# Optimization experiments

Measured on AMD Instinct MI355X. Metric: run time of the kernel, lower is better.

Reference implementation:

```python
import jax, jax.numpy as jnp
import numpy as np

B, S, D, L, H = 2, 2048, 2048, 3, 16
DH = D // H
BLOCK = 16
NA = 64
Q = NA * BLOCK
KV = S + Q
VOCAB = 32000
MASK_ID = 31999
GAMMA = 7.0
EPS = 1e-6


def _rope(x, pos):
    # x: [B,H,T,DH], pos: [B,T]
    half = DH // 2
    inv = 1.0 / (10000.0 ** (jnp.arange(half, dtype=jnp.float32) / half))
    ang = pos[:, None, :, None].astype(jnp.float32) * inv  # [B,1,T,half]
    c, s = jnp.cos(ang), jnp.sin(ang)
    x1, x2 = x[..., :half], x[..., half:]
    return jnp.concatenate([x1 * c - x2 * s, x2 * c + x1 * s], axis=-1)


def setup_inputs() -> dict:
    key = jax.random.key(0)
    ks = jax.random.split(key, 12)
    w = lambda k, shp: 0.02 * jax.random.normal(k, shp, jnp.float32)
    return {
        'input_ids': jax.random.randint(ks[0], (B, S), 0, VOCAB, dtype=jnp.int32),
        'hidden_states': jax.random.normal(ks[1], (L, B, S, D), jnp.float32),
        'loss_mask': jnp.ones((B, S), jnp.int32),
        'lm_head_weight': w(ks[2], (VOCAB, D)),
        'norm_weight': jnp.ones((D,), jnp.float32),
        'anchor_positions': jnp.sort(jax.random.randint(ks[3], (B, NA), 0, S - BLOCK, dtype=jnp.int32), axis=-1),
        'ctx_proj_w': w(ks[4], (D, L * D)),
        'embed_table': w(ks[5], (VOCAB, D)),
        'wq': w(ks[6], (D, D)),
        'wk': w(ks[7], (D, D)),
        'wv': w(ks[8], (D, D)),
        'wo': w(ks[9], (D, D)),
    }


def reference(input_ids, hidden_states, loss_mask, lm_head_weight, norm_weight,
              anchor_positions, ctx_proj_w, embed_table, wq, wk, wv, wo):
    # --- context feature: concat L target-layer hiddens, project to D ---
    ctx_cat = jnp.transpose(hidden_states, (1, 2, 0, 3)).reshape(B, S, L * D)
    ctx = jnp.einsum('bsf,df->bsd', ctx_cat, ctx_proj_w)

    # --- position ids (context: 0..S-1; draft block i starts at anchor_i) ---
    ctx_pos = jnp.broadcast_to(jnp.arange(S, dtype=jnp.int32), (B, S))
    draft_pos = (anchor_positions[:, :, None] + jnp.arange(BLOCK, dtype=jnp.int32)[None, None, :]).reshape(B, Q)

    # --- draft input (anchor token + MASKs) and labels ---
    off = jnp.arange(Q, dtype=jnp.int32) % BLOCK                       # [Q]
    anchor_per_tok = jnp.repeat(anchor_positions, BLOCK, axis=1)       # [B,Q]
    anchor_tok = jnp.take_along_axis(input_ids, anchor_positions, axis=1)
    draft_ids = jnp.where(off[None, :] == 0, jnp.repeat(anchor_tok, BLOCK, axis=1), MASK_ID)
    labels = jnp.where(off[None, :] == 0, -100,
                       jnp.take_along_axis(input_ids, anchor_per_tok + off[None, :], axis=1))

    # --- block-causal mask: [B,Q,KV] ---
    qi = jnp.arange(Q, dtype=jnp.int32)
    ki = jnp.arange(KV, dtype=jnp.int32)
    qb = qi // BLOCK                                                   # [Q]
    apos = anchor_positions[:, qb]                                     # [B,Q]
    ctx_vis = (ki[None, None, :] < S) & (ki[None, None, :] < apos[:, :, None])
    kb = (ki - S) // BLOCK
    draft_vis = (ki >= S)[None, :] & (qb[:, None] == kb[None, :])      # [Q,KV]
    mask = ctx_vis | draft_vis[None]                                   # [B,Q,KV]

    # --- single RoPE attention layer: draft queries over [context; draft] ---
    emb = embed_table[draft_ids]                                       # [B,Q,D]
    x_kv = jnp.concatenate([ctx, emb], axis=1)                         # [B,KV,D]
    pos_kv = jnp.concatenate([ctx_pos, draft_pos], axis=1)             # [B,KV]
    q = _rope((emb @ wq.T).reshape(B, Q, H, DH).transpose(0, 2, 1, 3), draft_pos)
    k = _rope((x_kv @ wk.T).reshape(B, KV, H, DH).transpose(0, 2, 1, 3), pos_kv)
    v = (x_kv @ wv.T).reshape(B, KV, H, DH).transpose(0, 2, 1, 3)
    scores = jnp.einsum('bhqd,bhkd->bhqk', q, k) / np.float32(np.sqrt(DH))
    scores = jnp.where(mask[:, None], scores, jnp.float32(-1e30))
    attn = jax.nn.softmax(scores, axis=-1)
    out = jnp.einsum('bhqk,bhkd->bhqd', attn, v).transpose(0, 2, 1, 3).reshape(B, Q, D) @ wo.T
    hidden = emb + out

    # --- RMSNorm + LM head ---
    hidden = hidden * jax.lax.rsqrt(jnp.mean(hidden * hidden, -1, keepdims=True) + EPS) * norm_weight
    logits = hidden @ lm_head_weight.T                                 # [B,Q,VOCAB]

    # --- decay-weighted CE loss + accuracy ---
    logp = jax.nn.log_softmax(logits, axis=-1)
    lab = jnp.where(labels < 0, 0, labels)
    nll = -jnp.take_along_axis(logp, lab[..., None], axis=-1)[..., 0]
    valid = labels != -100
    offf = off.astype(jnp.float32)
    decay = jnp.where(off == 0, 0.0, jnp.exp(-(offf - 1.0) / GAMMA))   # [Q]
    w = decay[None, :] * valid.astype(jnp.float32)
    loss = jnp.sum(nll * w) / jnp.maximum(jnp.sum(w), 1e-6)
    preds = jnp.argmax(logits, axis=-1).astype(labels.dtype)
    acc = jnp.sum((preds == labels) & valid) / jnp.maximum(jnp.sum(valid), 1)
    return loss, acc.astype(jnp.float32)
```

## Files before the change

### kernel.cpp

```cpp
#include <hip/hip_runtime.h>

#define B_ 2
#define S_ 2048
#define D_ 2048
#define L_ 3
#define H_ 16
#define DH_ 128
#define BLK_ 16
#define NA_ 64
#define Q_ 1024
#define KV_ 3072
#define VOCAB_ 32000
#define MASK_ID_ 31999
#define NTOK_ (B_*Q_)
#define VTILES_ (VOCAB_/128)

typedef __attribute__((ext_vector_type(8))) short bf16x8;
typedef __attribute__((ext_vector_type(4))) float f32x4;
typedef const __attribute__((address_space(1))) void* gptr_t;
typedef __attribute__((address_space(3))) void* lptr_t;

__device__ inline unsigned short f2bf(float x) {
  unsigned int u = __float_as_uint(x);
  unsigned int r = (u + 0x7fff + ((u >> 16) & 1)) >> 16;
  return (unsigned short)r;
}
__device__ inline float bf2f(unsigned short u) {
  return __uint_as_float(((unsigned int)u) << 16);
}

__global__ void k_meta(const int* __restrict__ ids, const int* __restrict__ anchors,
                       int* __restrict__ dids, int* __restrict__ dpos, int* __restrict__ labels) {
  int t = blockIdx.x * 256 + threadIdx.x;
  if (t >= NTOK_) return;
  int b = t >> 10, qi = t & 1023;
  int a = qi >> 4, off = qi & 15;
  int ap = anchors[b * NA_ + a];
  dpos[t] = ap + off;
  dids[t] = (off == 0) ? ids[b * S_ + ap] : MASK_ID_;
  labels[t] = (off == 0) ? -100 : ids[b * S_ + ap + off];
}

__global__ void k_cvt(const float* __restrict__ in, unsigned short* __restrict__ out, int n4) {
  int i = blockIdx.x * 256 + threadIdx.x;
  if (i >= n4) return;
  float4 v = ((const float4*)in)[i];
  ushort4 o;
  o.x = f2bf(v.x); o.y = f2bf(v.y); o.z = f2bf(v.z); o.w = f2bf(v.w);
  ((ushort4*)out)[i] = o;
}

__global__ void k_cvt_ctx(const float* __restrict__ hs, unsigned short* __restrict__ out) {
  int bi = blockIdx.x;
  int l = bi % 3, row = bi / 3;
  const float4* src = (const float4*)(hs + ((size_t)l * B_ * S_ + row) * (size_t)D_);
  ushort4* dst = (ushort4*)(out + (size_t)row * (3 * D_) + (size_t)l * D_);
  for (int i = threadIdx.x; i < D_ / 4; i += 256) {
    float4 v = src[i];
    ushort4 o;
    o.x = f2bf(v.x); o.y = f2bf(v.y); o.z = f2bf(v.z); o.w = f2bf(v.w);
    dst[i] = o;
  }
}

__global__ void k_gather(const float* __restrict__ table, const int* __restrict__ dids,
                         unsigned short* __restrict__ x_kv) {
  int row = blockIdx.x;
  int b = row >> 10, qi = row & 1023;
  const float4* src = (const float4*)(table + (size_t)dids[row] * D_);
  ushort4* dst = (ushort4*)(x_kv + ((size_t)b * KV_ + S_ + qi) * D_);
  for (int i = threadIdx.x; i < D_ / 4; i += 256) {
    float4 v = src[i];
    ushort4 o;
    o.x = f2bf(v.x); o.y = f2bf(v.y); o.z = f2bf(v.z); o.w = f2bf(v.w);
    dst[i] = o;
  }
}

template <int CMODE, int MAP>
__global__ __launch_bounds__(256) void k_mfma_bt(
    const unsigned short* __restrict__ A, const unsigned short* __restrict__ Bw,
    float* __restrict__ Cf, unsigned short* __restrict__ Cb,
    int M, int N, int K, int adivlog, long long abump, int cdivlog, long long cbump,
    const int* __restrict__ labels, float* __restrict__ pm, float* __restrict__ ps,
    int* __restrict__ pbi, float* __restrict__ plab) {
  __shared__ unsigned short As[128 * 32];
  __shared__ unsigned short Bs[128 * 32];
  int bx, by;
  if (MAP == 0) {
    int ntn = N >> 7;
    bx = blockIdx.x % ntn, by = blockIdx.x / ntn;
  } else {
    int per = gridDim.x >> 3;
    int wgid = (blockIdx.x & 7) * per + (blockIdx.x >> 3);
    int ntm = M >> 7;
    by = wgid % ntm, bx = wgid / ntm;
  }
  int rowbase = by << 7, colbase = bx << 7;
  int tid = threadIdx.x, lane = tid & 63, w = tid >> 6;
  int wr = w >> 1, wc = w & 1;
  int lo = lane & 15, hi = lane >> 4;

  f32x4 acc[4][4];
#pragma unroll
  for (int m = 0; m < 4; ++m)
#pragma unroll
    for (int n = 0; n < 4; ++n) acc[m][n] = (f32x4){0.f, 0.f, 0.f, 0.f};

  for (int kt = 0; kt < K; kt += 32) {
#pragma unroll
    for (int i = 0; i < 2; ++i) {
      int seg = i * 4 + w;
      int rloc = seg * 16 + (lane >> 2);
      int kcol = kt + ((lane & 3) << 3);
      int ra = rowbase + rloc;
      long long aoff = (long long)ra * K + (long long)(ra >> adivlog) * abump + kcol;
      __builtin_amdgcn_global_load_lds((gptr_t)(A + aoff), (lptr_t)(As + seg * 512), 16, 0, 0);
      int rb = colbase + rloc;
      long long boff = (long long)rb * K + kcol;
      __builtin_amdgcn_global_load_lds((gptr_t)(Bw + boff), (lptr_t)(Bs + seg * 512), 16, 0, 0);
    }
    __syncthreads();
    bf16x8 af[4], bfv[4];
#pragma unroll
    for (int m = 0; m < 4; ++m) {
      int row = wr * 64 + m * 16 + lo;
      af[m] = *(const bf16x8*)(As + row * 32 + (hi << 3));
    }
#pragma unroll
    for (int n = 0; n < 4; ++n) {
      int row = wc * 64 + n * 16 + lo;
      bfv[n] = *(const bf16x8*)(Bs + row * 32 + (hi << 3));
    }
#pragma unroll
    for (int m = 0; m < 4; ++m)
#pragma unroll
      for (int n = 0; n < 4; ++n)
        acc[m][n] = __builtin_amdgcn_mfma_f32_16x16x32_bf16(af[m], bfv[n], acc[m][n], 0, 0, 0);
    __syncthreads();
  }

  if (CMODE == 0 || CMODE == 1) {
#pragma unroll
    for (int m = 0; m < 4; ++m)
#pragma unroll
      for (int n = 0; n < 4; ++n)
#pragma unroll
        for (int r4 = 0; r4 < 4; ++r4) {
          int row = rowbase + wr * 64 + m * 16 + hi * 4 + r4;
          int col = colbase + wc * 64 + n * 16 + lo;
          size_t addr = (size_t)row * N + (size_t)(row >> cdivlog) * cbump + col;
          if (CMODE == 0) Cf[addr] = acc[m][n][r4];
          else Cb[addr] = f2bf(acc[m][n][r4]);
        }
  } else if (CMODE == 3) {
#pragma unroll
    for (int m = 0; m < 4; ++m)
#pragma unroll
      for (int n = 0; n < 4; ++n)
#pragma unroll
        for (int r4 = 0; r4 < 4; ++r4) {
          int row = rowbase + wr * 64 + m * 16 + hi * 4 + r4;
          int col = colbase + wc * 64 + n * 16 + lo;
          int bb = row >= KV_;
          int kv = row - bb * KV_;
          size_t addr = ((size_t)(bb * H_ + (col >> 7)) * 128 + (col & 127)) * KV_ + kv;
          Cb[addr] = f2bf(acc[m][n][r4]);
        }
  } else {
    float* f = (float*)As;
    int* ii = (int*)Bs;
    if (tid < 128) { f[640 + tid] = -3.0e38f; ii[256 + tid] = labels[rowbase + tid]; }
    __syncthreads();
#pragma unroll
    for (int m = 0; m < 4; ++m)
#pragma unroll
      for (int r4 = 0; r4 < 4; ++r4) {
        int trow = wr * 64 + m * 16 + hi * 4 + r4;
        float mx = acc[m][0][r4];
        int arg = colbase + wc * 64 + 0 * 16 + lo;
#pragma unroll
        for (int n = 1; n < 4; ++n) {
          float v = acc[m][n][r4];
          int c = colbase + wc * 64 + n * 16 + lo;
          if (v > mx || (v == mx && c < arg)) { mx = v; arg = c; }
        }
#pragma unroll
        for (int d = 1; d < 16; d <<= 1) {
          float om = __shfl_xor(mx, d);
          int oc = __shfl_xor(arg, d);
          if (om > mx || (om == mx && oc < arg)) { mx = om; arg = oc; }
        }
        if (lo == 0) { f[wc * 128 + trow] = mx; ii[wc * 128 + trow] = arg; }
      }
    __syncthreads();
    if (tid < 128) {
      float a = f[tid], b = f[128 + tid];
      int aa = ii[tid], bb = ii[128 + tid];
      float g; int ga;
      if (b > a || (b == a && bb < aa)) { g = b; ga = bb; } else { g = a; ga = aa; }
      f[512 + tid] = g; ii[384 + tid] = ga;
    }
    __syncthreads();
#pragma unroll
    for (int m = 0; m < 4; ++m)
#pragma unroll
      for (int r4 = 0; r4 < 4; ++r4) {
        int trow = wr * 64 + m * 16 + hi * 4 + r4;
        float gm = f[512 + trow];
        float s = 0.f;
#pragma unroll
        for (int n = 0; n < 4; ++n) s += __expf(acc[m][n][r4] - gm);
#pragma unroll
        for (int d = 1; d < 16; d <<= 1) s += __shfl_xor(s, d);
        if (lo == 0) f[256 + wc * 128 + trow] = s;
        int lab = ii[256 + trow];
        int rel = lab - colbase - wc * 64;
        if (rel >= 0 && rel < 64 && (rel & 15) == lo) {
#pragma unroll
          for (int n = 0; n < 4; ++n)
            if ((rel >> 4) == n) f[640 + trow] = acc[m][n][r4];
        }
      }
    __syncthreads();
    if (tid < 128) {
      int grow = rowbase + tid;
      size_t p = (size_t)grow * VTILES_ + bx;
      pm[p] = f[512 + tid];
      ps[p] = f[256 + tid] + f[256 + 128 + tid];
      pbi[p] = ii[384 + tid];
      plab[p] = f[640 + tid];
    }
  }
}

__global__ void k_rope(unsigned short* __restrict__ x, const int* __restrict__ dpos, int mode) {
  int idx = blockIdx.x * 256 + threadIdx.x;
  int j = idx & 63;
  int h = (idx >> 6) & 15;
  int row = idx >> 10;
  int pos;
  if (mode == 0) {
    if (row >= NTOK_) return;
    pos = dpos[row];
  } else {
    if (row >= B_ * KV_) return;
    int b = row / KV_, kvi = row % KV_;
    pos = (kvi < S_) ? kvi : dpos[b * Q_ + (kvi - S_)];
  }
  float inv = expf(-(float)j * (9.210340371976184f / 64.f));
  float ang = (float)pos * inv;
  float c = cosf(ang), s = sinf(ang);
  unsigned short* p = x + (size_t)row * D_ + h * DH_ + j;
  float x1 = bf2f(p[0]), x2 = bf2f(p[64]);
  p[0] = f2bf(x1 * c - x2 * s);
  p[64] = f2bf(x2 * c + x1 * s);
}

__global__ __launch_bounds__(256) void k_attn_mfma(
    const unsigned short* __restrict__ qb, const unsigned short* __restrict__ kb,
    const unsigned short* __restrict__ vt, const int* __restrict__ anchors,
    unsigned short* __restrict__ ob) {
  __shared__ __align__(16) unsigned short P_all[4][16 * 40];
  int w = threadIdx.x >> 6, lane = threadIdx.x & 63;
  int blk = blockIdx.x * 4 + w;
  int h = blk & 15, a = (blk >> 4) & 63, b = blk >> 10;
  int ql = lane & 15, p = lane >> 4;
  int apos = anchors[b * NA_ + a];
  unsigned short* P = P_all[w];

  const unsigned short* qbase = qb + ((size_t)(b * Q_ + a * 16 + ql)) * D_ + h * DH_;
  bf16x8 qf[4];
#pragma unroll
  for (int ks = 0; ks < 4; ++ks)
    qf[ks] = *(const bf16x8*)(qbase + ks * 32 + p * 8);

  const unsigned short* kbb = kb + (size_t)b * KV_ * D_ + h * DH_;
  const unsigned short* vtb = vt + ((size_t)(b * H_ + h)) * 128 * KV_;

  f32x4 o[8];
#pragma unroll
  for (int nt = 0; nt < 8; ++nt) o[nt] = (f32x4){0.f, 0.f, 0.f, 0.f};
  float mrun = -3.0e38f, lrun = 0.f;

  int ncx = (apos + 31) >> 5;
  const float scl = 0.08838834764831845f;

  for (int t = 0; t <= ncx; ++t) {
    int ktb = (t < ncx) ? (t << 5) : (S_ + a * 16);
    int rem = apos - (t << 5);
    int vc = (t < ncx) ? (rem < 32 ? rem : 32) : 16;
    float s[2][4];
#pragma unroll
    for (int g = 0; g < 2; ++g) {
      if (g * 16 < vc) {
        f32x4 accs = (f32x4){0.f, 0.f, 0.f, 0.f};
        const unsigned short* krow = kbb + (size_t)(ktb + g * 16 + ql) * D_;
#pragma unroll
        for (int ks = 0; ks < 4; ++ks) {
          bf16x8 kf = *(const bf16x8*)(krow + ks * 32 + p * 8);
          accs = __builtin_amdgcn_mfma_f32_16x16x32_bf16(kf, qf[ks], accs, 0, 0, 0);
        }
#pragma unroll
        for (int r = 0; r < 4; ++r) {
          int kl = g * 16 + p * 4 + r;
          s[g][r] = (kl < vc) ? accs[r] * scl : -3.0e38f;
        }
      } else {
#pragma unroll
        for (int r = 0; r < 4; ++r) s[g][r] = -3.0e38f;
      }
    }
    float mt = s[0][0];
#pragma unroll
    for (int g = 0; g < 2; ++g)
#pragma unroll
      for (int r = 0; r < 4; ++r) mt = fmaxf(mt, s[g][r]);
    mt = fmaxf(mt, __shfl_xor(mt, 16));
    mt = fmaxf(mt, __shfl_xor(mt, 32));
    float mnew = fmaxf(mrun, mt);
    float corr = __expf(mrun - mnew);
    float psum = 0.f;
#pragma unroll
    for (int g = 0; g < 2; ++g) {
      float p0 = __expf(s[g][0] - mnew), p1 = __expf(s[g][1] - mnew);
      float p2 = __expf(s[g][2] - mnew), p3 = __expf(s[g][3] - mnew);
      psum += p0 + p1 + p2 + p3;
      ushort2 w0, w1;
      w0.x = f2bf(p0); w0.y = f2bf(p1); w1.x = f2bf(p2); w1.y = f2bf(p3);
      int eo = ql * 40 + g * 16 + p * 4;
      *(ushort2*)(P + eo) = w0;
      *(ushort2*)(P + eo + 2) = w1;
    }
    psum += __shfl_xor(psum, 16);
    psum += __shfl_xor(psum, 32);
    lrun = lrun * corr + psum;
    mrun = mnew;
    float cr[4];
#pragma unroll
    for (int r = 0; r < 4; ++r) cr[r] = __shfl(corr, p * 4 + r);
#pragma unroll
    for (int nt = 0; nt < 8; ++nt)
#pragma unroll
      for (int r = 0; r < 4; ++r) o[nt][r] *= cr[r];
    bf16x8 pf = *(const bf16x8*)(P + ql * 40 + p * 8);
#pragma unroll
    for (int nt = 0; nt < 8; ++nt) {
      bf16x8 vf = *(const bf16x8*)(vtb + (size_t)(nt * 16 + ql) * KV_ + ktb + p * 8);
      o[nt] = __builtin_amdgcn_mfma_f32_16x16x32_bf16(pf, vf, o[nt], 0, 0, 0);
    }
  }
  float lq[4];
#pragma unroll
  for (int r = 0; r < 4; ++r) lq[r] = 1.f / __shfl(lrun, p * 4 + r);
  unsigned short* obase = ob + ((size_t)(b * Q_ + a * 16)) * D_ + h * DH_;
#pragma unroll
  for (int nt = 0; nt < 8; ++nt)
#pragma unroll
    for (int r = 0; r < 4; ++r)
      obase[(size_t)(p * 4 + r) * D_ + nt * 16 + ql] = f2bf(o[nt][r] * lq[r]);
}

__global__ void k_rmsnorm(const unsigned short* __restrict__ x_kv, const float* __restrict__ proj,
                          const float* __restrict__ nw, unsigned short* __restrict__ outp) {
  int row = blockIdx.x;
  int b = row >> 10, qi = row & 1023;
  const unsigned short* emb = x_kv + ((size_t)b * KV_ + S_ + qi) * D_;
  const float* pr = proj + (size_t)row * D_;
  __shared__ float red[256];
  float h[8];
  float ssum = 0.f;
#pragma unroll
  for (int i = 0; i < 8; ++i) {
    int d = threadIdx.x + i * 256;
    h[i] = bf2f(emb[d]) + pr[d];
    ssum += h[i] * h[i];
  }
  red[threadIdx.x] = ssum;
  __syncthreads();
  for (int s = 128; s; s >>= 1) {
    if (threadIdx.x < s) red[threadIdx.x] += red[threadIdx.x + s];
    __syncthreads();
  }
  float scale = rsqrtf(red[0] / (float)D_ + 1e-6f);
#pragma unroll
  for (int i = 0; i < 8; ++i) {
    int d = threadIdx.x + i * 256;
    outp[(size_t)row * D_ + d] = f2bf(h[i] * scale * nw[d]);
  }
}

__global__ void k_combine(const float* __restrict__ pm, const float* __restrict__ ps,
                          const int* __restrict__ pbi, const float* __restrict__ plab,
                          const int* __restrict__ labels, float* __restrict__ ts) {
  int t = blockIdx.x * 256 + threadIdx.x;
  if (t >= NTOK_) return;
  const float* pmr = pm + (size_t)t * VTILES_;
  const float* psr = ps + (size_t)t * VTILES_;
  const int* pbir = pbi + (size_t)t * VTILES_;
  const float* plabr = plab + (size_t)t * VTILES_;
  float M = -3.0e38f; int bi = 0;
  for (int x = 0; x < VTILES_; ++x) {
    float v = pmr[x];
    if (v > M) { M = v; bi = pbir[x]; }
  }
  float ssum = 0.f, labl = -3.0e38f;
  for (int x = 0; x < VTILES_; ++x) {
    ssum += psr[x] * __expf(pmr[x] - M);
    labl = fmaxf(labl, plabr[x]);
  }
  float lse = M + logf(ssum);
  int lab = labels[t];
  int off = t & 15;
  float valid = (lab != -100) ? 1.f : 0.f;
  float w = (off == 0) ? 0.f : __expf(-(float)(off - 1) / 7.0f);
  w *= valid;
  float nll = (lab != -100) ? (lse - labl) : 0.f;
  float correct = (valid > 0.f && bi == lab) ? 1.f : 0.f;
  ts[t * 4 + 0] = nll * w;
  ts[t * 4 + 1] = w;
  ts[t * 4 + 2] = correct;
  ts[t * 4 + 3] = valid;
}

__global__ void k_finalize(const float* __restrict__ ts, float* __restrict__ out) {
  __shared__ float r0[256], r1[256], r2[256], r3[256];
  int tid = threadIdx.x;
  float s0 = 0, s1 = 0, s2 = 0, s3 = 0;
  for (int t = tid; t < NTOK_; t += 256) {
    s0 += ts[t * 4 + 0]; s1 += ts[t * 4 + 1];
    s2 += ts[t * 4 + 2]; s3 += ts[t * 4 + 3];
  }
  r0[tid] = s0; r1[tid] = s1; r2[tid] = s2; r3[tid] = s3;
  __syncthreads();
  for (int s = 128; s; s >>= 1) {
    if (tid < s) {
      r0[tid] += r0[tid + s]; r1[tid] += r1[tid + s];
      r2[tid] += r2[tid + s]; r3[tid] += r3[tid + s];
    }
    __syncthreads();
  }
  if (tid == 0) {
    out[0] = r0[0] / fmaxf(r1[0], 1e-6f);
    out[1] = r2[0] / fmaxf(r3[0], 1.f);
  }
}

extern "C" void kernel_launch(void* const* d_in, const int* in_sizes, int n_in,
                              void* d_out, int out_size, void* d_ws, size_t ws_size,
                              hipStream_t stream) {
  const int* input_ids = (const int*)d_in[0];
  const float* hs = (const float*)d_in[1];
  const float* lm_head = (const float*)d_in[3];
  const float* norm_w = (const float*)d_in[4];
  const int* anchors = (const int*)d_in[5];
  const float* ctx_w = (const float*)d_in[6];
  const float* embed = (const float*)d_in[7];
  const float* wq = (const float*)d_in[8];
  const float* wk = (const float*)d_in[9];
  const float* wv = (const float*)d_in[10];
  const float* wo = (const float*)d_in[11];
  float* out = (float*)d_out;

  char* base = (char*)d_ws;
  size_t off = 0;
  unsigned short* x_kv_bf = (unsigned short*)(base + off); off += (size_t)B_ * KV_ * D_ * 2;
  unsigned short* wkb = (unsigned short*)(base + off); off += (size_t)D_ * D_ * 2;
  unsigned short* wvb = (unsigned short*)(base + off); off += (size_t)D_ * D_ * 2;
  unsigned short* wqb = (unsigned short*)(base + off); off += (size_t)D_ * D_ * 2;
  unsigned short* wob = (unsigned short*)(base + off); off += (size_t)D_ * D_ * 2;
  unsigned short* hidden_bf = (unsigned short*)(base + off); off += (size_t)NTOK_ * D_ * 2;
  unsigned short* attn_bf = (unsigned short*)(base + off); off += (size_t)NTOK_ * D_ * 2;
  float* proj = (float*)(base + off); off += (size_t)NTOK_ * D_ * 4;
  float* pm = (float*)(base + off); off += (size_t)NTOK_ * VTILES_ * 4;
  float* psum = (float*)(base + off); off += (size_t)NTOK_ * VTILES_ * 4;
  float* plab = (float*)(base + off); off += (size_t)NTOK_ * VTILES_ * 4;
  int* pbi = (int*)(base + off); off += (size_t)NTOK_ * VTILES_ * 4;
  float* tstats = (float*)(base + off); off += (size_t)NTOK_ * 4 * 4;
  int* dids = (int*)(base + off); off += NTOK_ * 4;
  int* dpos = (int*)(base + off); off += NTOK_ * 4;
  int* labels = (int*)(base + off); off += NTOK_ * 4;
  char* regA = base + off;
  const size_t SLACK = 65536;
  unsigned short* ctxA = (unsigned short*)(regA);
  unsigned short* ctx_wbf = (unsigned short*)(regA + 50331648);
  unsigned short* kbuf = (unsigned short*)(regA + 50331648 + 25165824);
  unsigned short* vtbuf = (unsigned short*)(regA + 50331648 + 2 * 25165824 + SLACK);
  unsigned short* qbuf = (unsigned short*)(regA + 50331648 + 3 * 25165824 + 2 * SLACK);
  unsigned short* lm_bf = (unsigned short*)(regA);

  k_meta<<<(NTOK_ + 255) / 256, 256, 0, stream>>>(input_ids, anchors, dids, dpos, labels);
  k_cvt<<<((D_ * (L_ * D_) / 4) + 255) / 256, 256, 0, stream>>>(ctx_w, ctx_wbf, D_ * (L_ * D_) / 4);
  k_cvt<<<((D_ * D_ / 4) + 255) / 256, 256, 0, stream>>>(wk, wkb, D_ * D_ / 4);
  k_cvt<<<((D_ * D_ / 4) + 255) / 256, 256, 0, stream>>>(wv, wvb, D_ * D_ / 4);
  k_cvt<<<((D_ * D_ / 4) + 255) / 256, 256, 0, stream>>>(wq, wqb, D_ * D_ / 4);
  k_cvt<<<((D_ * D_ / 4) + 255) / 256, 256, 0, stream>>>(wo, wob, D_ * D_ / 4);
  k_cvt_ctx<<<B_ * S_ * L_, 256, 0, stream>>>(hs, ctxA);
  k_gather<<<NTOK_, 256, 0, stream>>>(embed, dids, x_kv_bf);

  k_mfma_bt<1, 0><<<(4096 / 128) * (2048 / 128), 256, 0, stream>>>(
      ctxA, ctx_wbf, nullptr, x_kv_bf, 4096, 2048, 6144, 30, 0LL, 11, (long long)Q_ * D_,
      nullptr, nullptr, nullptr, nullptr, nullptr);
  k_mfma_bt<1, 0><<<(6144 / 128) * (2048 / 128), 256, 0, stream>>>(
      x_kv_bf, wkb, nullptr, kbuf, 6144, 2048, 2048, 30, 0LL, 30, 0LL,
      nullptr, nullptr, nullptr, nullptr, nullptr);
  k_mfma_bt<3, 0><<<(6144 / 128) * (2048 / 128), 256, 0, stream>>>(
      x_kv_bf, wvb, nullptr, vtbuf, 6144, 2048, 2048, 30, 0LL, 30, 0LL,
      nullptr, nullptr, nullptr, nullptr, nullptr);
  k_mfma_bt<1, 0><<<(2048 / 128) * (2048 / 128), 256, 0, stream>>>(
      x_kv_bf + (size_t)S_ * D_, wqb, nullptr, qbuf, 2048, 2048, 2048, 10,
      (long long)(KV_ - Q_) * D_, 30, 0LL,
      nullptr, nullptr, nullptr, nullptr, nullptr);
  k_rope<<<(NTOK_ * H_ * 64) / 256, 256, 0, stream>>>(qbuf, dpos, 0);
  k_rope<<<(B_ * KV_ * H_ * 64) / 256, 256, 0, stream>>>(kbuf, dpos, 1);
  k_attn_mfma<<<(B_ * NA_ * H_) / 4, 256, 0, stream>>>(qbuf, kbuf, vtbuf, anchors, attn_bf);
  k_mfma_bt<0, 0><<<(2048 / 128) * (2048 / 128), 256, 0, stream>>>(
      attn_bf, wob, proj, nullptr, 2048, 2048, 2048, 30, 0LL, 30, 0LL,
      nullptr, nullptr, nullptr, nullptr, nullptr);
  k_rmsnorm<<<NTOK_, 256, 0, stream>>>(x_kv_bf, proj, norm_w, hidden_bf);
  k_cvt<<<((VOCAB_ * D_ / 4) + 255) / 256, 256, 0, stream>>>(lm_head, lm_bf, VOCAB_ * D_ / 4);
  k_mfma_bt<2, 1><<<(2048 / 128) * (VOCAB_ / 128), 256, 0, stream>>>(
      hidden_bf, lm_bf, nullptr, nullptr, 2048, VOCAB_, 2048, 30, 0LL, 30, 0LL,
      labels, pm, psum, pbi, plab);
  k_combine<<<(NTOK_ + 255) / 256, 256, 0, stream>>>(pm, psum, pbi, plab, labels, tstats);
  k_finalize<<<1, 256, 0, stream>>>(tstats, out);
}
```

Measured before the change: 1.374 ms.

## Split attention over context into four chunks with a separate combine kernel

Replaces the single-pass per-(batch, anchor, head) attention with a split-KV (flash-decoding style) scheme. Each wave handles one 512-position context chunk, with the draft block attached to the last chunk, and writes partial max, sum and unnormalized output in fp32. A new combine kernel merges the four partials. The goal is more parallelism and less load imbalance from variable anchor lengths, at the cost of an extra launch and fp32 partial-output traffic through scratch memory that reuses the lm_bf region.

```diff
diff --git a/kernel.cpp b/kernel.cpp
--- a/kernel.cpp
+++ b/kernel.cpp
@@ -14,6 +14,7 @@
 #define MASK_ID_ 31999
 #define NTOK_ (B_*Q_)
 #define VTILES_ (VOCAB_/128)
+#define NCHUNK_ 4
 
 typedef __attribute__((ext_vector_type(8))) short bf16x8;
 typedef __attribute__((ext_vector_type(4))) float f32x4;
@@ -257,16 +258,27 @@
   p[64] = f2bf(x2 * c + x1 * s);
 }
 
-__global__ __launch_bounds__(256) void k_attn_mfma(
+__global__ __launch_bounds__(256) void k_attn_part(
     const unsigned short* __restrict__ qb, const unsigned short* __restrict__ kb,
     const unsigned short* __restrict__ vt, const int* __restrict__ anchors,
-    unsigned short* __restrict__ ob) {
+    float* __restrict__ pm_att, float* __restrict__ pl_att, float* __restrict__ po_att) {
   __shared__ __align__(16) unsigned short P_all[4][16 * 40];
   int w = threadIdx.x >> 6, lane = threadIdx.x & 63;
   int blk = blockIdx.x * 4 + w;
-  int h = blk & 15, a = (blk >> 4) & 63, b = blk >> 10;
+  int chunk = blk & 3, h = (blk >> 2) & 15, a = (blk >> 6) & 63, b = blk >> 12;
   int ql = lane & 15, p = lane >> 4;
   int apos = anchors[b * NA_ + a];
+
+  int cstart = chunk << 9;
+  int cend = min(apos, cstart + 512);
+  int len = (cend > cstart) ? (cend - cstart) : 0;
+  int ntile = (len + 31) >> 5;
+  int total = ntile + ((chunk == 3) ? 1 : 0);
+
+  if (total == 0) {
+    if (p == 0) { pm_att[blk * 16 + ql] = -3.0e38f; pl_att[blk * 16 + ql] = 0.f; }
+    return;
+  }
   unsigned short* P = P_all[w];
 
   const unsigned short* qbase = qb + ((size_t)(b * Q_ + a * 16 + ql)) * D_ + h * DH_;
@@ -282,14 +294,12 @@
 #pragma unroll
   for (int nt = 0; nt < 8; ++nt) o[nt] = (f32x4){0.f, 0.f, 0.f, 0.f};
   float mrun = -3.0e38f, lrun = 0.f;
-
-  int ncx = (apos + 31) >> 5;
   const float scl = 0.08838834764831845f;
 
-  for (int t = 0; t <= ncx; ++t) {
-    int ktb = (t < ncx) ? (t << 5) : (S_ + a * 16);
-    int rem = apos - (t << 5);
-    int vc = (t < ncx) ? (rem < 32 ? rem : 32) : 16;
+  for (int t = 0; t < total; ++t) {
+    bool isdraft = (chunk == 3) && (t == ntile);
+    int ktb = isdraft ? (S_ + a * 16) : (cstart + (t << 5));
+    int vc = isdraft ? 16 : min(32, cend - ktb);
     float s[2][4];
 #pragma unroll
     for (int g = 0; g < 2; ++g) {
@@ -350,15 +360,38 @@
       o[nt] = __builtin_amdgcn_mfma_f32_16x16x32_bf16(pf, vf, o[nt], 0, 0, 0);
     }
   }
-  float lq[4];
-#pragma unroll
-  for (int r = 0; r < 4; ++r) lq[r] = 1.f / __shfl(lrun, p * 4 + r);
-  unsigned short* obase = ob + ((size_t)(b * Q_ + a * 16)) * D_ + h * DH_;
+  if (p == 0) { pm_att[blk * 16 + ql] = mrun; pl_att[blk * 16 + ql] = lrun; }
+  float* pob = po_att + (size_t)blk * 2048;
 #pragma unroll
   for (int nt = 0; nt < 8; ++nt)
 #pragma unroll
     for (int r = 0; r < 4; ++r)
-      obase[(size_t)(p * 4 + r) * D_ + nt * 16 + ql] = f2bf(o[nt][r] * lq[r]);
+      pob[(p * 4 + r) * 128 + nt * 16 + ql] = o[nt][r];
+}
+
+__global__ __launch_bounds__(256) void k_attn_combine(
+    const float* __restrict__ pm_att, const float* __restrict__ pl_att,
+    const float* __restrict__ po_att, unsigned short* __restrict__ ob) {
+  int base = blockIdx.x;
+  int h = base & 15, a = (base >> 4) & 63, b = base >> 10;
+  int d = threadIdx.x & 127, qh = threadIdx.x >> 7;
+  int pbase = base * 4;
+#pragma unroll
+  for (int qq = 0; qq < 8; ++qq) {
+    int q = qh * 8 + qq;
+    float m0 = pm_att[(pbase + 0) * 16 + q], m1 = pm_att[(pbase + 1) * 16 + q];
+    float m2 = pm_att[(pbase + 2) * 16 + q], m3 = pm_att[(pbase + 3) * 16 + q];
+    float mg = fmaxf(fmaxf(m0, m1), fmaxf(m2, m3));
+    float w0 = __expf(m0 - mg), w1 = __expf(m1 - mg);
+    float w2 = __expf(m2 - mg), w3 = __expf(m3 - mg);
+    float lg = pl_att[(pbase + 0) * 16 + q] * w0 + pl_att[(pbase + 1) * 16 + q] * w1 +
+               pl_att[(pbase + 2) * 16 + q] * w2 + pl_att[(pbase + 3) * 16 + q] * w3;
+    float od = po_att[(size_t)(pbase + 0) * 2048 + q * 128 + d] * w0 +
+               po_att[(size_t)(pbase + 1) * 2048 + q * 128 + d] * w1 +
+               po_att[(size_t)(pbase + 2) * 2048 + q * 128 + d] * w2 +
+               po_att[(size_t)(pbase + 3) * 2048 + q * 128 + d] * w3;
+    ob[((size_t)(b * Q_ + a * 16 + q)) * D_ + h * DH_ + d] = f2bf(od / lg);
+  }
 }
 
 __global__ void k_rmsnorm(const unsigned short* __restrict__ x_kv, const float* __restrict__ proj,
@@ -488,6 +521,9 @@
   unsigned short* vtbuf = (unsigned short*)(regA + 50331648 + 2 * 25165824 + SLACK);
   unsigned short* qbuf = (unsigned short*)(regA + 50331648 + 3 * 25165824 + 2 * SLACK);
   unsigned short* lm_bf = (unsigned short*)(regA);
+  float* po_att = (float*)(regA);
+  float* pm_att = (float*)(regA + 67108864);
+  float* pl_att = (float*)(regA + 67108864 + 524288);
 
   k_meta<<<(NTOK_ + 255) / 256, 256, 0, stream>>>(input_ids, anchors, dids, dpos, labels);
   k_cvt<<<((D_ * (L_ * D_) / 4) + 255) / 256, 256, 0, stream>>>(ctx_w, ctx_wbf, D_ * (L_ * D_) / 4);
@@ -513,7 +549,9 @@
       nullptr, nullptr, nullptr, nullptr, nullptr);
   k_rope<<<(NTOK_ * H_ * 64) / 256, 256, 0, stream>>>(qbuf, dpos, 0);
   k_rope<<<(B_ * KV_ * H_ * 64) / 256, 256, 0, stream>>>(kbuf, dpos, 1);
-  k_attn_mfma<<<(B_ * NA_ * H_) / 4, 256, 0, stream>>>(qbuf, kbuf, vtbuf, anchors, attn_bf);
+  k_attn_part<<<(B_ * NA_ * H_ * NCHUNK_) / 4, 256, 0, stream>>>(
+      qbuf, kbuf, vtbuf, anchors, pm_att, pl_att, po_att);
+  k_attn_combine<<<B_ * NA_ * H_, 256, 0, stream>>>(pm_att, pl_att, po_att, attn_bf);
   k_mfma_bt<0, 0><<<(2048 / 128) * (2048 / 128), 256, 0, stream>>>(
       attn_bf, wob, proj, nullptr, 2048, 2048, 2048, 30, 0LL, 30, 0LL,
       nullptr, nullptr, nullptr, nullptr, nullptr);
```

Result: faster. 1.312 ms (-4.5%).
